# Performance work log

Measured on AMD Instinct MI355X. Metric: run time of the kernel, lower is better.

## Reference

```python
import jax, jax.numpy as jnp
import numpy as np

T, N, E = 8, 10000, 200000
F_IN, H, OUT = 32, 128, 64
EPS = 1e-5


def setup_inputs() -> dict:
    key = jax.random.key(0)
    ks = jax.random.split(key, 28)
    inp = {}
    inp['x'] = jax.random.normal(ks[0], (T, N, F_IN), jnp.float32)
    inp['edge_index'] = jax.random.randint(ks[1], (2, E), 0, N, dtype=jnp.int32)
    # GCN layer weights (Glorot-ish scale)
    inp['w_gcn0'] = jax.random.normal(ks[2], (F_IN, H), jnp.float32) / np.float32(np.sqrt(F_IN))
    inp['b_gcn0'] = jnp.zeros((H,), jnp.float32)
    inp['w_gcn1'] = jax.random.normal(ks[3], (H, H), jnp.float32) / np.float32(np.sqrt(H))
    inp['b_gcn1'] = jnp.zeros((H,), jnp.float32)
    inp['w_gcn2'] = jax.random.normal(ks[4], (H, H), jnp.float32) / np.float32(np.sqrt(H))
    inp['b_gcn2'] = jnp.zeros((H,), jnp.float32)
    # BatchNorm (eval mode) params for the two inner norms
    for i, kb in zip(range(2), range(5, 9, 2)):
        inp[f'bn_g{i}'] = 1.0 + 0.1 * jax.random.normal(ks[kb], (H,), jnp.float32)
        inp[f'bn_b{i}'] = 0.1 * jax.random.normal(ks[kb + 1], (H,), jnp.float32)
        inp[f'bn_m{i}'] = 0.1 * jax.random.normal(ks[kb + 10], (H,), jnp.float32)
        inp[f'bn_v{i}'] = jax.random.uniform(ks[kb + 11], (H,), jnp.float32, 0.5, 1.5)
    # 3-layer LSTM params, torch gate order (i, f, g, o)
    s = np.float32(1.0 / np.sqrt(OUT))
    dims_in = [H, OUT, OUT]
    for l in range(3):
        k0, k1, k2, k3 = jax.random.split(ks[20 + l], 4)
        inp[f'w_ih_{l}'] = jax.random.uniform(k0, (4 * OUT, dims_in[l]), jnp.float32, -s, s)
        inp[f'w_hh_{l}'] = jax.random.uniform(k1, (4 * OUT, OUT), jnp.float32, -s, s)
        inp[f'b_ih_{l}'] = jax.random.uniform(k2, (4 * OUT,), jnp.float32, -s, s)
        inp[f'b_hh_{l}'] = jax.random.uniform(k3, (4 * OUT,), jnp.float32, -s, s)
    return inp


def reference(x, edge_index, w_gcn0, b_gcn0, w_gcn1, b_gcn1, w_gcn2, b_gcn2,
              bn_g0, bn_b0, bn_m0, bn_v0, bn_g1, bn_b1, bn_m1, bn_v1,
              w_ih_0, w_hh_0, b_ih_0, b_hh_0,
              w_ih_1, w_hh_1, b_ih_1, b_hh_1,
              w_ih_2, w_hh_2, b_ih_2, b_hh_2):
    src, dst = edge_index[0], edge_index[1]
    # symmetric GCN normalization with self-loops: deg = in-degree + 1
    deg = jax.ops.segment_sum(jnp.ones((E,), x.dtype), dst, num_segments=N) + 1.0
    dis = jax.lax.rsqrt(deg)
    coef = dis[src] * dis[dst]          # [E] edge norm
    self_w = dis * dis                   # [N] self-loop norm

    def gcn(h, W, b):
        hw = jnp.einsum('tnf,fo->tno', h, W)                      # [T,N,O]
        msg = hw[:, src, :] * coef[None, :, None]                  # [T,E,O]
        agg = jax.vmap(lambda m: jax.ops.segment_sum(m, dst, num_segments=N))(msg)
        return agg + hw * self_w[None, :, None] + b

    def bn(h, g, b_, m, v):  # eval-mode BatchNorm1d
        return (h - m) * (g * jax.lax.rsqrt(v + EPS)) + b_

    h = bn(jax.nn.relu(gcn(x, w_gcn0, b_gcn0)), bn_g0, bn_b0, bn_m0, bn_v0)
    h = bn(jax.nn.relu(gcn(h, w_gcn1, b_gcn1)), bn_g1, bn_b1, bn_m1, bn_v1)
    h = jax.nn.relu(gcn(h, w_gcn2, b_gcn2))                        # [T,N,H]

    def lstm_layer(xs, Wih, Whh, bih, bhh):
        Hd = Whh.shape[1]
        bias = bih + bhh
        def step(carry, xt):
            hp, cp = carry
            g = xt @ Wih.T + hp @ Whh.T + bias
            i, f, gg, o = jnp.split(g, 4, axis=-1)
            c = jax.nn.sigmoid(f) * cp + jax.nn.sigmoid(i) * jnp.tanh(gg)
            hn = jax.nn.sigmoid(o) * jnp.tanh(c)
            return (hn, c), hn
        z = jnp.zeros((xs.shape[1], Hd), xs.dtype)
        _, ys = jax.lax.scan(step, (z, z), xs)
        return ys  # [T,N,Hd]

    ys = lstm_layer(h, w_ih_0, w_hh_0, b_ih_0, b_hh_0)
    ys = lstm_layer(ys, w_ih_1, w_hh_1, b_ih_1, b_hh_1)
    ys = lstm_layer(ys, w_ih_2, w_hh_2, b_ih_2, b_hh_2)
    return ys[-1]  # [N, OUT] == x[:, -1, :] in the torch code
```

## Files before the change

kernel.cpp:

```cpp
#include <hip/hip_runtime.h>
#include <hip/hip_bf16.h>
#include <math.h>

#define NTHREADS 256
#define T_STEPS 8
#define F_INC 32
#define H_DIM 128
#define O_DIM 64

typedef unsigned short u16;
typedef __attribute__((ext_vector_type(8))) short short8_t;
typedef __attribute__((ext_vector_type(4))) float float4_t;
typedef __attribute__((ext_vector_type(2))) float float2_t;

__device__ __forceinline__ float bf2f(u16 u) {
    return __uint_as_float(((unsigned)u) << 16);
}
__device__ __forceinline__ u16 f2bf(float f) {
    __hip_bfloat16 h = __float2bfloat16(f);
    union { __hip_bfloat16 h; u16 s; } cv; cv.h = h; return cv.s;
}
__device__ __forceinline__ float2_t bfpair(unsigned u) {
    union { unsigned w[2]; float2_t f; } c;
    c.w[0] = u << 16;
    c.w[1] = u & 0xffff0000u;
    return c.f;
}
__device__ __forceinline__ void bf8_unpack(uint4 u, float* f) {
    f[0] = __uint_as_float(u.x << 16); f[1] = __uint_as_float(u.x & 0xffff0000u);
    f[2] = __uint_as_float(u.y << 16); f[3] = __uint_as_float(u.y & 0xffff0000u);
    f[4] = __uint_as_float(u.z << 16); f[5] = __uint_as_float(u.z & 0xffff0000u);
    f[6] = __uint_as_float(u.w << 16); f[7] = __uint_as_float(u.w & 0xffff0000u);
}
__device__ __forceinline__ float fsig(float x) {
    float xc = fminf(fmaxf(x, -30.f), 30.f);
    float e = __builtin_amdgcn_exp2f(xc * -1.4426950408889634f);
    return __builtin_amdgcn_rcpf(1.0f + e);
}
__device__ __forceinline__ float ftanh(float x) {
    float xc = fminf(fmaxf(x, -15.f), 15.f);
    float e = __builtin_amdgcn_exp2f(xc * -2.8853900817779268f);
    float r = __builtin_amdgcn_rcpf(1.0f + e);
    return fmaf(-2.0f * e, r, 1.0f);
}

__global__ void count_wprep_kernel(const int* __restrict__ ei, int* __restrict__ cnt,
                                   int E, int gE,
                                   const float* g0, const float* g1, const float* g2,
                                   const float* i0, const float* i1, const float* i2,
                                   const float* h0, const float* h1, const float* h2,
                                   u16* o_g0, u16* o_g1, u16* o_g2,
                                   u16* o_i0, u16* o_i1, u16* o_i2,
                                   u16* o_h0, u16* o_h1, u16* o_h2) {
    if ((int)blockIdx.x < gE) {
        int e = blockIdx.x * NTHREADS + threadIdx.x;
        if (e < E) atomicAdd(&cnt[ei[E + e]], 1);
        return;
    }
    const int i = (blockIdx.x - gE) * NTHREADS + threadIdx.x;
    if (i < 4096)        { o_g0[i] = f2bf(g0[(i & 31) * 128 + (i >> 5)]); }
    else if (i < 20480)  { int j = i - 4096;   o_g1[j] = f2bf(g1[(j & 127) * 128 + (j >> 7)]); }
    else if (i < 36864)  { int j = i - 20480;  o_g2[j] = f2bf(g2[(j & 127) * 128 + (j >> 7)]); }
    else if (i < 69632)  { int j = i - 36864;  o_i0[j] = f2bf(i0[j]); }
    else if (i < 86016)  { int j = i - 69632;  o_i1[j] = f2bf(i1[j]); }
    else if (i < 102400) { int j = i - 86016;  o_i2[j] = f2bf(i2[j]); }
    else if (i < 118784) { int j = i - 102400; o_h0[j] = f2bf(h0[j]); }
    else if (i < 135168) { int j = i - 118784; o_h1[j] = f2bf(h1[j]); }
    else if (i < 151552) { int j = i - 135168; o_h2[j] = f2bf(h2[j]); }
}

__global__ void scan_part1(const int* __restrict__ cnt, int* __restrict__ bsum, int n) {
    __shared__ int sd[NTHREADS];
    const int i = blockIdx.x * NTHREADS + threadIdx.x;
    sd[threadIdx.x] = (i < n) ? cnt[i] : 0;
    __syncthreads();
    for (int off = 128; off > 0; off >>= 1) {
        if (threadIdx.x < off) sd[threadIdx.x] += sd[threadIdx.x + off];
        __syncthreads();
    }
    if (threadIdx.x == 0) bsum[blockIdx.x] = sd[0];
}

__global__ void scan_part3(const int* __restrict__ cnt, const int* __restrict__ bsum,
                           int* __restrict__ rowptr, int* __restrict__ wp,
                           float* __restrict__ dis, float* __restrict__ selfw, int n) {
    __shared__ int sd[NTHREADS];
    __shared__ int sbase;
    const int tid = threadIdx.x;
    if (tid < 64) {
        int v0 = (tid < blockIdx.x) ? bsum[tid] : 0;
        #pragma unroll
        for (int off = 1; off < 64; off <<= 1) v0 += __shfl_xor(v0, off);
        if (tid == 0) sbase = v0;
    }
    const int i = blockIdx.x * NTHREADS + tid;
    const int v = (i < n) ? cnt[i] : 0;
    sd[tid] = v;
    __syncthreads();
    for (int off = 1; off < NTHREADS; off <<= 1) {
        const int tv = (tid >= off) ? sd[tid - off] : 0;
        __syncthreads();
        sd[tid] += tv;
        __syncthreads();
    }
    const int excl = sbase + sd[tid] - v;
    if (i < n) {
        rowptr[i] = excl; wp[i] = excl;
        if (i == n - 1) rowptr[n] = excl + v;
        const float d = 1.0f + (float)v;
        dis[i] = rsqrtf(d);
        selfw[i] = 1.0f / d;
    }
}

__global__ void fill_kernel(const int* __restrict__ ei, const float* __restrict__ dis,
                            int* __restrict__ wp, int2* __restrict__ epk, int E) {
    int e = blockIdx.x * NTHREADS + threadIdx.x;
    if (e < E) {
        int s = ei[e], d = ei[E + e];
        int p = atomicAdd(&wp[d], 1);
        epk[p] = make_int2(s, __float_as_int(dis[s] * dis[d]));
    }
}

__global__ __launch_bounds__(NTHREADS)
void gcn32_kernel(const float* __restrict__ x, const int* __restrict__ rowptr,
                  const int2* __restrict__ epk,
                  const float* __restrict__ selfw, const u16* __restrict__ Wt,
                  const float* __restrict__ bias,
                  const float* __restrict__ bng, const float* __restrict__ bnb,
                  const float* __restrict__ bnm, const float* __restrict__ bnv,
                  u16* __restrict__ out, int N) {
    constexpr int ASTR = 40;
    constexpr int ECAP = 1024;
    __shared__ __align__(16) u16 aT[2][16][ASTR];
    __shared__ int2 sM[ECAP];
    const int t0 = blockIdx.x * 2;
    const int n0 = blockIdx.y * 16;
    const int tid = threadIdx.x;
    const int wid = tid >> 6, lane = tid & 63;
    const int quad = lane >> 4, l16 = lane & 15;
    const float* xb0 = x + (long)t0 * N * 32;
    const float* xb1 = xb0 + (long)N * 32;

    const int eb0 = rowptr[n0];
    const int ecnt = min(rowptr[n0 + 16] - eb0, ECAP);
    for (int p = tid; p < ecnt; p += NTHREADS) sM[p] = epk[eb0 + p];
    __syncthreads();

    const int split = lane >> 3;
    const int c4 = (lane & 7) * 4;
    for (int i = 0; i < 4; ++i) {
        const int n = n0 + wid * 4 + i;
        const int l0 = rowptr[n] - eb0;
        const int l1 = rowptr[n + 1] - eb0;
        const int eL = min(l1, ecnt);
        const int start = l0 + split;
        float2_t a0[2] = {(float2_t){0.f, 0.f}, (float2_t){0.f, 0.f}};
        float2_t a1[2] = {(float2_t){0.f, 0.f}, (float2_t){0.f, 0.f}};
        #pragma unroll 2
        for (int e = start; e < eL; e += 8) {
            const int2 m = sM[e];
            const float w = __int_as_float(m.y);
            const float2_t w2 = {w, w};
            const long o = (long)m.x * 32 + c4;
            const float4 v0 = *(const float4*)(xb0 + o);
            const float4 v1 = *(const float4*)(xb1 + o);
            a0[0] = __builtin_elementwise_fma((float2_t){v0.x, v0.y}, w2, a0[0]);
            a0[1] = __builtin_elementwise_fma((float2_t){v0.z, v0.w}, w2, a0[1]);
            a1[0] = __builtin_elementwise_fma((float2_t){v1.x, v1.y}, w2, a1[0]);
            a1[1] = __builtin_elementwise_fma((float2_t){v1.z, v1.w}, w2, a1[1]);
        }
        const int kL = (eL > start) ? (eL - start + 7) >> 3 : 0;
        for (int e = start + kL * 8; e < l1; e += 8) {
            const int2 m = epk[eb0 + e];
            const float w = __int_as_float(m.y);
            const float2_t w2 = {w, w};
            const long o = (long)m.x * 32 + c4;
            const float4 v0 = *(const float4*)(xb0 + o);
            const float4 v1 = *(const float4*)(xb1 + o);
            a0[0] = __builtin_elementwise_fma((float2_t){v0.x, v0.y}, w2, a0[0]);
            a0[1] = __builtin_elementwise_fma((float2_t){v0.z, v0.w}, w2, a0[1]);
            a1[0] = __builtin_elementwise_fma((float2_t){v1.x, v1.y}, w2, a1[0]);
            a1[1] = __builtin_elementwise_fma((float2_t){v1.z, v1.w}, w2, a1[1]);
        }
        float r[8] = {a0[0][0], a0[0][1], a0[1][0], a0[1][1],
                      a1[0][0], a1[0][1], a1[1][0], a1[1][1]};
        #pragma unroll
        for (int j = 0; j < 8; ++j) {
            r[j] += __shfl_xor(r[j], 8);
            r[j] += __shfl_xor(r[j], 16);
            r[j] += __shfl_xor(r[j], 32);
        }
        if (split == 0) {
            const float sw = selfw[n];
            const float4 s0 = *(const float4*)(xb0 + (long)n * 32 + c4);
            const float4 s1 = *(const float4*)(xb1 + (long)n * 32 + c4);
            ushort4 o0, o1;
            o0.x = f2bf(fmaf(sw, s0.x, r[0])); o0.y = f2bf(fmaf(sw, s0.y, r[1]));
            o0.z = f2bf(fmaf(sw, s0.z, r[2])); o0.w = f2bf(fmaf(sw, s0.w, r[3]));
            o1.x = f2bf(fmaf(sw, s1.x, r[4])); o1.y = f2bf(fmaf(sw, s1.y, r[5]));
            o1.z = f2bf(fmaf(sw, s1.z, r[6])); o1.w = f2bf(fmaf(sw, s1.w, r[7]));
            *(ushort4*)(&aT[0][wid * 4 + i][c4]) = o0;
            *(ushort4*)(&aT[1][wid * 4 + i][c4]) = o1;
        }
    }
    __syncthreads();

    const short8_t fA0 = *(const short8_t*)(&aT[0][l16][quad * 8]);
    const short8_t fA1 = *(const short8_t*)(&aT[1][l16][quad * 8]);
    float4_t acc[2][2];
    short8_t fB[2];
    #pragma unroll
    for (int ct = 0; ct < 2; ++ct) {
        const int col = wid * 32 + ct * 16 + l16;
        fB[ct] = *(const short8_t*)(Wt + (long)col * 32 + quad * 8);
        acc[0][ct] = (float4_t){0.f, 0.f, 0.f, 0.f};
        acc[1][ct] = (float4_t){0.f, 0.f, 0.f, 0.f};
    }
    #pragma unroll
    for (int ct = 0; ct < 2; ++ct) {
        acc[0][ct] = __builtin_amdgcn_mfma_f32_16x16x32_bf16(fA0, fB[ct], acc[0][ct], 0, 0, 0);
        acc[1][ct] = __builtin_amdgcn_mfma_f32_16x16x32_bf16(fA1, fB[ct], acc[1][ct], 0, 0, 0);
    }

    #pragma unroll
    for (int ct = 0; ct < 2; ++ct) {
        const int c = wid * 32 + ct * 16 + l16;
        const float s = bng[c] * rsqrtf(bnv[c] + 1e-5f);
        const float a1 = bnb[c] - bnm[c] * s;
        const float a0 = bias[c];
        #pragma unroll
        for (int tt = 0; tt < 2; ++tt) {
            #pragma unroll
            for (int r = 0; r < 4; ++r) {
                const int node = quad * 4 + r;
                float v = fmaf(fmaxf(acc[tt][ct][r] + a0, 0.f), s, a1);
                out[((long)(t0 + tt) * N + n0 + node) * 128 + c] = f2bf(v);
            }
        }
    }
}

template<int EPI>
__global__ __launch_bounds__(NTHREADS)
void gcn128_kernel(const u16* __restrict__ h, const int* __restrict__ rowptr,
                   const int2* __restrict__ epk,
                   const float* __restrict__ selfw, const u16* __restrict__ Wt,
                   const float* __restrict__ bias,
                   const float* __restrict__ bng, const float* __restrict__ bnb,
                   const float* __restrict__ bnm, const float* __restrict__ bnv,
                   u16* __restrict__ out, int N) {
    constexpr int ASTR = 136;
    constexpr int ECAP = 1024;
    __shared__ __align__(16) u16 aT[2][16][ASTR];
    __shared__ int2 sM[ECAP];
    const int t0 = blockIdx.x * 2;
    const int n0 = blockIdx.y * 16;
    const int tid = threadIdx.x;
    const int wid = tid >> 6, lane = tid & 63;
    const int quad = lane >> 4, l16 = lane & 15;
    const u16* hb0 = h + (long)t0 * N * 128;
    const u16* hb1 = hb0 + (long)N * 128;

    const int eb0 = rowptr[n0];
    const int ecnt = min(rowptr[n0 + 16] - eb0, ECAP);
    for (int p = tid; p < ecnt; p += NTHREADS) sM[p] = epk[eb0 + p];
    __syncthreads();

    const int split = lane >> 4;
    const int c8 = l16 * 8;
    for (int i = 0; i < 4; ++i) {
        const int n = n0 + wid * 4 + i;
        const int l0 = rowptr[n] - eb0;
        const int l1 = rowptr[n + 1] - eb0;
        const int eL = min(l1, ecnt);
        const int start = l0 + split;
        float2_t aA[4] = {(float2_t){0.f, 0.f}, (float2_t){0.f, 0.f},
                          (float2_t){0.f, 0.f}, (float2_t){0.f, 0.f}};
        float2_t aB[4] = {(float2_t){0.f, 0.f}, (float2_t){0.f, 0.f},
                          (float2_t){0.f, 0.f}, (float2_t){0.f, 0.f}};
        #pragma unroll 4
        for (int e = start; e < eL; e += 4) {
            const int2 m = sM[e];
            const float w = __int_as_float(m.y);
            const float2_t w2 = {w, w};
            const long o = (long)m.x * 128 + c8;
            const uint4 v0 = *(const uint4*)(hb0 + o);
            const uint4 v1 = *(const uint4*)(hb1 + o);
            aA[0] = __builtin_elementwise_fma(bfpair(v0.x), w2, aA[0]);
            aA[1] = __builtin_elementwise_fma(bfpair(v0.y), w2, aA[1]);
            aA[2] = __builtin_elementwise_fma(bfpair(v0.z), w2, aA[2]);
            aA[3] = __builtin_elementwise_fma(bfpair(v0.w), w2, aA[3]);
            aB[0] = __builtin_elementwise_fma(bfpair(v1.x), w2, aB[0]);
            aB[1] = __builtin_elementwise_fma(bfpair(v1.y), w2, aB[1]);
            aB[2] = __builtin_elementwise_fma(bfpair(v1.z), w2, aB[2]);
            aB[3] = __builtin_elementwise_fma(bfpair(v1.w), w2, aB[3]);
        }
        const int kL = (eL > start) ? (eL - start + 3) >> 2 : 0;
        for (int e = start + kL * 4; e < l1; e += 4) {
            const int2 m = epk[eb0 + e];
            const float w = __int_as_float(m.y);
            const float2_t w2 = {w, w};
            const long o = (long)m.x * 128 + c8;
            const uint4 v0 = *(const uint4*)(hb0 + o);
            const uint4 v1 = *(const uint4*)(hb1 + o);
            aA[0] = __builtin_elementwise_fma(bfpair(v0.x), w2, aA[0]);
            aA[1] = __builtin_elementwise_fma(bfpair(v0.y), w2, aA[1]);
            aA[2] = __builtin_elementwise_fma(bfpair(v0.z), w2, aA[2]);
            aA[3] = __builtin_elementwise_fma(bfpair(v0.w), w2, aA[3]);
            aB[0] = __builtin_elementwise_fma(bfpair(v1.x), w2, aB[0]);
            aB[1] = __builtin_elementwise_fma(bfpair(v1.y), w2, aB[1]);
            aB[2] = __builtin_elementwise_fma(bfpair(v1.z), w2, aB[2]);
            aB[3] = __builtin_elementwise_fma(bfpair(v1.w), w2, aB[3]);
        }
        float a[16] = {aA[0][0], aA[0][1], aA[1][0], aA[1][1],
                       aA[2][0], aA[2][1], aA[3][0], aA[3][1],
                       aB[0][0], aB[0][1], aB[1][0], aB[1][1],
                       aB[2][0], aB[2][1], aB[3][0], aB[3][1]};
        #pragma unroll
        for (int j = 0; j < 16; ++j) {
            a[j] += __shfl_xor(a[j], 16);
            a[j] += __shfl_xor(a[j], 32);
        }
        if (split == 0) {
            const float sw = selfw[n];
            const uint4 s0 = *(const uint4*)(hb0 + (long)n * 128 + c8);
            const uint4 s1 = *(const uint4*)(hb1 + (long)n * 128 + c8);
            float f0[8], f1[8];
            bf8_unpack(s0, f0);
            bf8_unpack(s1, f1);
            ushort4 oA0, oA1, oB0, oB1;
            oA0.x = f2bf(fmaf(sw, f0[0], a[0]));  oA0.y = f2bf(fmaf(sw, f0[1], a[1]));
            oA0.z = f2bf(fmaf(sw, f0[2], a[2]));  oA0.w = f2bf(fmaf(sw, f0[3], a[3]));
            oA1.x = f2bf(fmaf(sw, f0[4], a[4]));  oA1.y = f2bf(fmaf(sw, f0[5], a[5]));
            oA1.z = f2bf(fmaf(sw, f0[6], a[6]));  oA1.w = f2bf(fmaf(sw, f0[7], a[7]));
            oB0.x = f2bf(fmaf(sw, f1[0], a[8]));  oB0.y = f2bf(fmaf(sw, f1[1], a[9]));
            oB0.z = f2bf(fmaf(sw, f1[2], a[10])); oB0.w = f2bf(fmaf(sw, f1[3], a[11]));
            oB1.x = f2bf(fmaf(sw, f1[4], a[12])); oB1.y = f2bf(fmaf(sw, f1[5], a[13]));
            oB1.z = f2bf(fmaf(sw, f1[6], a[14])); oB1.w = f2bf(fmaf(sw, f1[7], a[15]));
            *(ushort4*)(&aT[0][wid * 4 + i][c8]) = oA0;
            *(ushort4*)(&aT[0][wid * 4 + i][c8 + 4]) = oA1;
            *(ushort4*)(&aT[1][wid * 4 + i][c8]) = oB0;
            *(ushort4*)(&aT[1][wid * 4 + i][c8 + 4]) = oB1;
        }
    }
    __syncthreads();

    short8_t fA0[4], fA1[4];
    #pragma unroll
    for (int ks = 0; ks < 4; ++ks) {
        fA0[ks] = *(const short8_t*)(&aT[0][l16][ks * 32 + quad * 8]);
        fA1[ks] = *(const short8_t*)(&aT[1][l16][ks * 32 + quad * 8]);
    }
    float4_t acc[2][2];
    #pragma unroll
    for (int tt = 0; tt < 2; ++tt)
        #pragma unroll
        for (int ct = 0; ct < 2; ++ct) acc[tt][ct] = (float4_t){0.f, 0.f, 0.f, 0.f};
    #pragma unroll
    for (int ct = 0; ct < 2; ++ct) {
        const int col = wid * 32 + ct * 16 + l16;
        #pragma unroll
        for (int ks = 0; ks < 4; ++ks) {
            const short8_t fB = *(const short8_t*)(Wt + (long)col * 128 + ks * 32 + quad * 8);
            acc[0][ct] = __builtin_amdgcn_mfma_f32_16x16x32_bf16(fA0[ks], fB, acc[0][ct], 0, 0, 0);
            acc[1][ct] = __builtin_amdgcn_mfma_f32_16x16x32_bf16(fA1[ks], fB, acc[1][ct], 0, 0, 0);
        }
    }

    #pragma unroll
    for (int ct = 0; ct < 2; ++ct) {
        const int c = wid * 32 + ct * 16 + l16;
        const float a0 = bias[c];
        float s = 0.f, a1 = 0.f;
        if constexpr (EPI == 2) {
            s = bng[c] * rsqrtf(bnv[c] + 1e-5f);
            a1 = bnb[c] - bnm[c] * s;
        }
        #pragma unroll
        for (int tt = 0; tt < 2; ++tt) {
            #pragma unroll
            for (int r = 0; r < 4; ++r) {
                const int node = quad * 4 + r;
                float v = fmaxf(acc[tt][ct][r] + a0, 0.f);
                if constexpr (EPI == 2) v = fmaf(v, s, a1);
                out[((long)(t0 + tt) * N + n0 + node) * 128 + c] = f2bf(v);
            }
        }
    }
}

__global__ __launch_bounds__(NTHREADS, 2)
void lstm0_kernel(const u16* __restrict__ in_h, const u16* __restrict__ wih,
                  const u16* __restrict__ whh,
                  const float* __restrict__ bi, const float* __restrict__ bh,
                  u16* __restrict__ out_hi, u16* __restrict__ out_lo, int N) {
    constexpr int HSTR = 76;
    const int tid = threadIdx.x;
    const int w = tid >> 6, lane = tid & 63;
    const int quad = lane >> 4, l16 = lane & 15;
    const int n0 = blockIdx.x * 16;
    const int u = w * 16 + l16;

    __shared__ __align__(16) u16 hT[2][16][HSTR];
    for (int p = tid; p < 2 * 16 * HSTR; p += NTHREADS) (&hT[0][0][0])[p] = 0;

    short8_t fI[4][4], fH[4][2];
    #pragma unroll
    for (int g = 0; g < 4; ++g) {
        #pragma unroll
        for (int ks = 0; ks < 4; ++ks)
            fI[g][ks] = *(const short8_t*)(wih + (long)(g * 64 + u) * 128 + ks * 32 + quad * 8);
        #pragma unroll
        for (int ks = 0; ks < 2; ++ks)
            fH[g][ks] = *(const short8_t*)(whh + (long)(g * 64 + u) * 64 + ks * 32 + quad * 8);
    }
    float bias[4];
    #pragma unroll
    for (int g = 0; g < 4; ++g) bias[g] = bi[g * 64 + u] + bh[g * 64 + u];
    float cst[4] = {};
    __syncthreads();

    #pragma unroll 1
    for (int t = 0; t < T_STEPS; ++t) {
        short8_t ain[4];
        const long ibase = ((long)t * N + n0 + l16) * 128 + quad * 8;
        #pragma unroll
        for (int ks = 0; ks < 4; ++ks)
            ain[ks] = *(const short8_t*)(in_h + ibase + ks * 32);
        short8_t ah[2], al[2];
        #pragma unroll
        for (int ks = 0; ks < 2; ++ks) {
            ah[ks] = *(const short8_t*)(&hT[0][l16][ks * 32 + quad * 8]);
            al[ks] = *(const short8_t*)(&hT[1][l16][ks * 32 + quad * 8]);
        }
        __syncthreads();

        float4_t acc[4];
        #pragma unroll
        for (int g = 0; g < 4; ++g) acc[g] = (float4_t){bias[g], bias[g], bias[g], bias[g]};
        #pragma unroll
        for (int ks = 0; ks < 4; ++ks)
            #pragma unroll
            for (int g = 0; g < 4; ++g)
                acc[g] = __builtin_amdgcn_mfma_f32_16x16x32_bf16(ain[ks], fI[g][ks], acc[g], 0, 0, 0);
        #pragma unroll
        for (int ks = 0; ks < 2; ++ks)
            #pragma unroll
            for (int g = 0; g < 4; ++g) {
                acc[g] = __builtin_amdgcn_mfma_f32_16x16x32_bf16(ah[ks], fH[g][ks], acc[g], 0, 0, 0);
                acc[g] = __builtin_amdgcn_mfma_f32_16x16x32_bf16(al[ks], fH[g][ks], acc[g], 0, 0, 0);
            }

        #pragma unroll
        for (int r = 0; r < 4; ++r) {
            const float si = fsig(acc[0][r]);
            const float sf = fsig(acc[1][r]);
            const float gg = ftanh(acc[2][r]);
            const float so = fsig(acc[3][r]);
            const float c = sf * cst[r] + si * gg;
            cst[r] = c;
            const float h = so * ftanh(c);
            const int node = quad * 4 + r;
            const u16 hi = f2bf(h);
            const u16 lo = f2bf(h - bf2f(hi));
            hT[0][node][u] = hi;
            hT[1][node][u] = lo;
            const long o = ((long)t * N + n0 + node) * 64 + u;
            out_hi[o] = hi;
            out_lo[o] = lo;
        }
        __syncthreads();
    }
}

__global__ __launch_bounds__(NTHREADS)
void lstm12_kernel(const u16* __restrict__ in_hi, const u16* __restrict__ in_lo,
                   const u16* __restrict__ wih1, const u16* __restrict__ whh1,
                   const u16* __restrict__ wih2, const u16* __restrict__ whh2,
                   const float* __restrict__ bi1, const float* __restrict__ bh1,
                   const float* __restrict__ bi2, const float* __restrict__ bh2,
                   float* __restrict__ out_f, int N) {
    constexpr int HSTR = 76;
    const int tid = threadIdx.x;
    const int w = tid >> 6, lane = tid & 63;
    const int quad = lane >> 4, l16 = lane & 15;
    const int n0 = blockIdx.x * 16;
    const int u = w * 16 + l16;

    __shared__ __align__(16) u16 hT[2][2][16][HSTR];
    for (int p = tid; p < 2 * 2 * 16 * HSTR; p += NTHREADS) (&hT[0][0][0][0])[p] = 0;

    short8_t fI1[4][2], fH1[4][2], fI2[4][2], fH2[4][2];
    #pragma unroll
    for (int g = 0; g < 4; ++g)
        #pragma unroll
        for (int ks = 0; ks < 2; ++ks) {
            fI1[g][ks] = *(const short8_t*)(wih1 + (long)(g * 64 + u) * 64 + ks * 32 + quad * 8);
            fH1[g][ks] = *(const short8_t*)(whh1 + (long)(g * 64 + u) * 64 + ks * 32 + quad * 8);
            fI2[g][ks] = *(const short8_t*)(wih2 + (long)(g * 64 + u) * 64 + ks * 32 + quad * 8);
            fH2[g][ks] = *(const short8_t*)(whh2 + (long)(g * 64 + u) * 64 + ks * 32 + quad * 8);
        }
    float b1[4], b2[4];
    #pragma unroll
    for (int g = 0; g < 4; ++g) {
        b1[g] = bi1[g * 64 + u] + bh1[g * 64 + u];
        b2[g] = bi2[g * 64 + u] + bh2[g * 64 + u];
    }
    float c1[4] = {}, c2[4] = {};
    __syncthreads();

    #pragma unroll 1
    for (int t = 0; t < T_STEPS; ++t) {
        short8_t ainh[2], ainl[2], r1h[2], r1l[2], r2h[2], r2l[2];
        const long ibase = ((long)t * N + n0 + l16) * 64 + quad * 8;
        #pragma unroll
        for (int ks = 0; ks < 2; ++ks) {
            ainh[ks] = *(const short8_t*)(in_hi + ibase + ks * 32);
            ainl[ks] = *(const short8_t*)(in_lo + ibase + ks * 32);
            r1h[ks] = *(const short8_t*)(&hT[0][0][l16][ks * 32 + quad * 8]);
            r1l[ks] = *(const short8_t*)(&hT[0][1][l16][ks * 32 + quad * 8]);
            r2h[ks] = *(const short8_t*)(&hT[1][0][l16][ks * 32 + quad * 8]);
            r2l[ks] = *(const short8_t*)(&hT[1][1][l16][ks * 32 + quad * 8]);
        }
        __syncthreads();

        float4_t acc[4];
        #pragma unroll
        for (int g = 0; g < 4; ++g) acc[g] = (float4_t){b1[g], b1[g], b1[g], b1[g]};
        #pragma unroll
        for (int ks = 0; ks < 2; ++ks)
            #pragma unroll
            for (int g = 0; g < 4; ++g) {
                acc[g] = __builtin_amdgcn_mfma_f32_16x16x32_bf16(ainh[ks], fI1[g][ks], acc[g], 0, 0, 0);
                acc[g] = __builtin_amdgcn_mfma_f32_16x16x32_bf16(ainl[ks], fI1[g][ks], acc[g], 0, 0, 0);
                acc[g] = __builtin_amdgcn_mfma_f32_16x16x32_bf16(r1h[ks], fH1[g][ks], acc[g], 0, 0, 0);
                acc[g] = __builtin_amdgcn_mfma_f32_16x16x32_bf16(r1l[ks], fH1[g][ks], acc[g], 0, 0, 0);
            }
        #pragma unroll
        for (int r = 0; r < 4; ++r) {
            const float si = fsig(acc[0][r]);
            const float sf = fsig(acc[1][r]);
            const float gg = ftanh(acc[2][r]);
            const float so = fsig(acc[3][r]);
            const float c = sf * c1[r] + si * gg;
            c1[r] = c;
            const float h = so * ftanh(c);
            const int node = quad * 4 + r;
            const u16 hi = f2bf(h);
            hT[0][0][node][u] = hi;
            hT[0][1][node][u] = f2bf(h - bf2f(hi));
        }
        __syncthreads();

        short8_t i2h[2], i2l[2];
        #pragma unroll
        for (int ks = 0; ks < 2; ++ks) {
            i2h[ks] = *(const short8_t*)(&hT[0][0][l16][ks * 32 + quad * 8]);
            i2l[ks] = *(const short8_t*)(&hT[0][1][l16][ks * 32 + quad * 8]);
        }
        #pragma unroll
        for (int g = 0; g < 4; ++g) acc[g] = (float4_t){b2[g], b2[g], b2[g], b2[g]};
        #pragma unroll
        for (int ks = 0; ks < 2; ++ks)
            #pragma unroll
            for (int g = 0; g < 4; ++g) {
                acc[g] = __builtin_amdgcn_mfma_f32_16x16x32_bf16(i2h[ks], fI2[g][ks], acc[g], 0, 0, 0);
                acc[g] = __builtin_amdgcn_mfma_f32_16x16x32_bf16(i2l[ks], fI2[g][ks], acc[g], 0, 0, 0);
                acc[g] = __builtin_amdgcn_mfma_f32_16x16x32_bf16(r2h[ks], fH2[g][ks], acc[g], 0, 0, 0);
                acc[g] = __builtin_amdgcn_mfma_f32_16x16x32_bf16(r2l[ks], fH2[g][ks], acc[g], 0, 0, 0);
            }
        #pragma unroll
        for (int r = 0; r < 4; ++r) {
            const float si = fsig(acc[0][r]);
            const float sf = fsig(acc[1][r]);
            const float gg = ftanh(acc[2][r]);
            const float so = fsig(acc[3][r]);
            const float c = sf * c2[r] + si * gg;
            c2[r] = c;
            const float h = so * ftanh(c);
            const int node = quad * 4 + r;
            if (t == T_STEPS - 1) {
                out_f[(long)(n0 + node) * 64 + u] = h;
            } else {
                const u16 hi = f2bf(h);
                hT[1][0][node][u] = hi;
                hT[1][1][node][u] = f2bf(h - bf2f(hi));
            }
        }
        __syncthreads();
    }
}

extern "C" void kernel_launch(void* const* d_in, const int* in_sizes, int n_in,
                              void* d_out, int out_size, void* d_ws, size_t ws_size,
                              hipStream_t stream) {
    (void)n_in; (void)out_size; (void)ws_size;
    const float* x      = (const float*)d_in[0];
    const int*   ei     = (const int*)d_in[1];
    const float* w_gcn0 = (const float*)d_in[2];
    const float* b_gcn0 = (const float*)d_in[3];
    const float* w_gcn1 = (const float*)d_in[4];
    const float* b_gcn1 = (const float*)d_in[5];
    const float* w_gcn2 = (const float*)d_in[6];
    const float* b_gcn2 = (const float*)d_in[7];
    const float* bn_g0  = (const float*)d_in[8];
    const float* bn_b0  = (const float*)d_in[9];
    const float* bn_m0  = (const float*)d_in[10];
    const float* bn_v0  = (const float*)d_in[11];
    const float* bn_g1  = (const float*)d_in[12];
    const float* bn_b1  = (const float*)d_in[13];
    const float* bn_m1  = (const float*)d_in[14];
    const float* bn_v1  = (const float*)d_in[15];
    const float* w_ih_0 = (const float*)d_in[16];
    const float* w_hh_0 = (const float*)d_in[17];
    const float* b_ih_0 = (const float*)d_in[18];
    const float* b_hh_0 = (const float*)d_in[19];
    const float* w_ih_1 = (const float*)d_in[20];
    const float* w_hh_1 = (const float*)d_in[21];
    const float* b_ih_1 = (const float*)d_in[22];
    const float* b_hh_1 = (const float*)d_in[23];
    const float* w_ih_2 = (const float*)d_in[24];
    const float* w_hh_2 = (const float*)d_in[25];
    const float* b_ih_2 = (const float*)d_in[26];
    const float* b_hh_2 = (const float*)d_in[27];

    const int E = in_sizes[1] / 2;
    const int N = in_sizes[0] / (T_STEPS * F_INC);
    const long M = (long)N * T_STEPS;

    char* ws = (char*)d_ws;
    size_t off = 0;
    auto carve = [&](size_t bytes) -> void* {
        void* p = ws + off;
        off += (bytes + 255) & ~(size_t)255;
        return p;
    };
    float* dis     = (float*)carve((size_t)N * 4);
    float* selfw   = (float*)carve((size_t)N * 4);
    int*   cnt     = (int*)carve((size_t)N * 4);
    int*   rowptr  = (int*)carve((size_t)(N + 1) * 4);
    int*   wp      = (int*)carve((size_t)N * 4);
    int2*  epk     = (int2*)carve((size_t)E * 8);
    int*   bsum    = (int*)carve(64 * 4);
    u16*   hbuf    = (u16*)carve((size_t)M * H_DIM * 2);
    u16*   hbuf2   = (u16*)carve((size_t)M * H_DIM * 2);
    u16*   pA_hi   = (u16*)carve((size_t)M * O_DIM * 2);
    u16*   pA_lo   = (u16*)carve((size_t)M * O_DIM * 2);
    u16*   wt0     = (u16*)carve((size_t)128 * 32 * 2);
    u16*   wt1     = (u16*)carve((size_t)128 * 128 * 2);
    u16*   wt2     = (u16*)carve((size_t)128 * 128 * 2);
    u16*   wtih0   = (u16*)carve((size_t)256 * 128 * 2);
    u16*   wtih1   = (u16*)carve((size_t)256 * 64 * 2);
    u16*   wtih2   = (u16*)carve((size_t)256 * 64 * 2);
    u16*   whh0b   = (u16*)carve((size_t)256 * 64 * 2);
    u16*   whh1b   = (u16*)carve((size_t)256 * 64 * 2);
    u16*   whh2b   = (u16*)carve((size_t)256 * 64 * 2);

    const dim3 b256(NTHREADS);
    const int gN = (N + NTHREADS - 1) / NTHREADS;
    const int gE = (E + NTHREADS - 1) / NTHREADS;

    hipMemsetAsync(cnt, 0, (size_t)N * 4, stream);
    count_wprep_kernel<<<gE + (151552 + 255) / 256, b256, 0, stream>>>(
        ei, cnt, E, gE,
        w_gcn0, w_gcn1, w_gcn2, w_ih_0, w_ih_1, w_ih_2, w_hh_0, w_hh_1, w_hh_2,
        wt0, wt1, wt2, wtih0, wtih1, wtih2, whh0b, whh1b, whh2b);
    scan_part1<<<gN, b256, 0, stream>>>(cnt, bsum, N);
    scan_part3<<<gN, b256, 0, stream>>>(cnt, bsum, rowptr, wp, dis, selfw, N);
    fill_kernel<<<gE, b256, 0, stream>>>(ei, dis, wp, epk, E);

    const dim3 gG(T_STEPS / 2, N / 16);
    gcn32_kernel<<<gG, b256, 0, stream>>>(
        x, rowptr, epk, selfw, wt0, b_gcn0,
        bn_g0, bn_b0, bn_m0, bn_v0, hbuf, N);
    gcn128_kernel<2><<<gG, b256, 0, stream>>>(
        hbuf, rowptr, epk, selfw, wt1, b_gcn1,
        bn_g1, bn_b1, bn_m1, bn_v1, hbuf2, N);
    gcn128_kernel<1><<<gG, b256, 0, stream>>>(
        hbuf2, rowptr, epk, selfw, wt2, b_gcn2,
        nullptr, nullptr, nullptr, nullptr, hbuf, N);

    const int gL = N / 16;
    lstm0_kernel<<<gL, b256, 0, stream>>>(
        hbuf, wtih0, whh0b, b_ih_0, b_hh_0, pA_hi, pA_lo, N);
    lstm12_kernel<<<gL, b256, 0, stream>>>(
        pA_hi, pA_lo, wtih1, whh1b, wtih2, whh2b,
        b_ih_1, b_hh_1, b_ih_2, b_hh_2, (float*)d_out, N);
}
```

Measured before the change: 363.8 us.

## Convert x to bf16 upfront and split gcn128 blocks to one timestep

The prep kernel gains extra blocks that convert the fp32 input x to bf16, so the first GCN layer gathers half as many bytes per neighbor, and its gather loop unroll goes from 2 to 4. The 128-wide GCN kernels now handle one timestep per block instead of two, doubling the grid and halving per-thread registers and accumulators to raise occupancy and parallelism. The costs are an extra pass over x with a new workspace buffer, bf16 rounding of the raw input, and edge metadata that is now loaded twice as often in the 128-wide layers.

```diff
diff --git a/kernel.cpp b/kernel.cpp
--- a/kernel.cpp
+++ b/kernel.cpp
@@ -45,7 +45,8 @@
 }
 
 __global__ void count_wprep_kernel(const int* __restrict__ ei, int* __restrict__ cnt,
-                                   int E, int gE,
+                                   int E, int gE, int NX,
+                                   const float* __restrict__ x, u16* __restrict__ xb,
                                    const float* g0, const float* g1, const float* g2,
                                    const float* i0, const float* i1, const float* i2,
                                    const float* h0, const float* h1, const float* h2,
@@ -57,16 +58,26 @@
         if (e < E) atomicAdd(&cnt[ei[E + e]], 1);
         return;
     }
-    const int i = (blockIdx.x - gE) * NTHREADS + threadIdx.x;
-    if (i < 4096)        { o_g0[i] = f2bf(g0[(i & 31) * 128 + (i >> 5)]); }
-    else if (i < 20480)  { int j = i - 4096;   o_g1[j] = f2bf(g1[(j & 127) * 128 + (j >> 7)]); }
-    else if (i < 36864)  { int j = i - 20480;  o_g2[j] = f2bf(g2[(j & 127) * 128 + (j >> 7)]); }
-    else if (i < 69632)  { int j = i - 36864;  o_i0[j] = f2bf(i0[j]); }
-    else if (i < 86016)  { int j = i - 69632;  o_i1[j] = f2bf(i1[j]); }
-    else if (i < 102400) { int j = i - 86016;  o_i2[j] = f2bf(i2[j]); }
-    else if (i < 118784) { int j = i - 102400; o_h0[j] = f2bf(h0[j]); }
-    else if (i < 135168) { int j = i - 118784; o_h1[j] = f2bf(h1[j]); }
-    else if (i < 151552) { int j = i - 135168; o_h2[j] = f2bf(h2[j]); }
+    if ((int)blockIdx.x < gE + 592) {
+        const int i = (blockIdx.x - gE) * NTHREADS + threadIdx.x;
+        if (i < 4096)        { o_g0[i] = f2bf(g0[(i & 31) * 128 + (i >> 5)]); }
+        else if (i < 20480)  { int j = i - 4096;   o_g1[j] = f2bf(g1[(j & 127) * 128 + (j >> 7)]); }
+        else if (i < 36864)  { int j = i - 20480;  o_g2[j] = f2bf(g2[(j & 127) * 128 + (j >> 7)]); }
+        else if (i < 69632)  { int j = i - 36864;  o_i0[j] = f2bf(i0[j]); }
+        else if (i < 86016)  { int j = i - 69632;  o_i1[j] = f2bf(i1[j]); }
+        else if (i < 102400) { int j = i - 86016;  o_i2[j] = f2bf(i2[j]); }
+        else if (i < 118784) { int j = i - 102400; o_h0[j] = f2bf(h0[j]); }
+        else if (i < 135168) { int j = i - 118784; o_h1[j] = f2bf(h1[j]); }
+        else if (i < 151552) { int j = i - 135168; o_h2[j] = f2bf(h2[j]); }
+        return;
+    }
+    const long i4 = ((long)(blockIdx.x - gE - 592) * NTHREADS + threadIdx.x) * 4;
+    if (i4 < (long)NX) {
+        const float4 v = *(const float4*)(x + i4);
+        ushort4 o;
+        o.x = f2bf(v.x); o.y = f2bf(v.y); o.z = f2bf(v.z); o.w = f2bf(v.w);
+        *(ushort4*)(xb + i4) = o;
+    }
 }
 
 __global__ void scan_part1(const int* __restrict__ cnt, int* __restrict__ bsum, int n) {
@@ -124,7 +135,7 @@
 }
 
 __global__ __launch_bounds__(NTHREADS)
-void gcn32_kernel(const float* __restrict__ x, const int* __restrict__ rowptr,
+void gcn32_kernel(const u16* __restrict__ xb, const int* __restrict__ rowptr,
                   const int2* __restrict__ epk,
                   const float* __restrict__ selfw, const u16* __restrict__ Wt,
                   const float* __restrict__ bias,
@@ -140,8 +151,8 @@
     const int tid = threadIdx.x;
     const int wid = tid >> 6, lane = tid & 63;
     const int quad = lane >> 4, l16 = lane & 15;
-    const float* xb0 = x + (long)t0 * N * 32;
-    const float* xb1 = xb0 + (long)N * 32;
+    const u16* xb0 = xb + (long)t0 * N * 32;
+    const u16* xb1 = xb0 + (long)N * 32;
 
     const int eb0 = rowptr[n0];
     const int ecnt = min(rowptr[n0 + 16] - eb0, ECAP);
@@ -158,18 +169,18 @@
         const int start = l0 + split;
         float2_t a0[2] = {(float2_t){0.f, 0.f}, (float2_t){0.f, 0.f}};
         float2_t a1[2] = {(float2_t){0.f, 0.f}, (float2_t){0.f, 0.f}};
-        #pragma unroll 2
+        #pragma unroll 4
         for (int e = start; e < eL; e += 8) {
             const int2 m = sM[e];
             const float w = __int_as_float(m.y);
             const float2_t w2 = {w, w};
             const long o = (long)m.x * 32 + c4;
-            const float4 v0 = *(const float4*)(xb0 + o);
-            const float4 v1 = *(const float4*)(xb1 + o);
-            a0[0] = __builtin_elementwise_fma((float2_t){v0.x, v0.y}, w2, a0[0]);
-            a0[1] = __builtin_elementwise_fma((float2_t){v0.z, v0.w}, w2, a0[1]);
-            a1[0] = __builtin_elementwise_fma((float2_t){v1.x, v1.y}, w2, a1[0]);
-            a1[1] = __builtin_elementwise_fma((float2_t){v1.z, v1.w}, w2, a1[1]);
+            const uint2 v0 = *(const uint2*)(xb0 + o);
+            const uint2 v1 = *(const uint2*)(xb1 + o);
+            a0[0] = __builtin_elementwise_fma(bfpair(v0.x), w2, a0[0]);
+            a0[1] = __builtin_elementwise_fma(bfpair(v0.y), w2, a0[1]);
+            a1[0] = __builtin_elementwise_fma(bfpair(v1.x), w2, a1[0]);
+            a1[1] = __builtin_elementwise_fma(bfpair(v1.y), w2, a1[1]);
         }
         const int kL = (eL > start) ? (eL - start + 7) >> 3 : 0;
         for (int e = start + kL * 8; e < l1; e += 8) {
@@ -177,12 +188,12 @@
             const float w = __int_as_float(m.y);
             const float2_t w2 = {w, w};
             const long o = (long)m.x * 32 + c4;
-            const float4 v0 = *(const float4*)(xb0 + o);
-            const float4 v1 = *(const float4*)(xb1 + o);
-            a0[0] = __builtin_elementwise_fma((float2_t){v0.x, v0.y}, w2, a0[0]);
-            a0[1] = __builtin_elementwise_fma((float2_t){v0.z, v0.w}, w2, a0[1]);
-            a1[0] = __builtin_elementwise_fma((float2_t){v1.x, v1.y}, w2, a1[0]);
-            a1[1] = __builtin_elementwise_fma((float2_t){v1.z, v1.w}, w2, a1[1]);
+            const uint2 v0 = *(const uint2*)(xb0 + o);
+            const uint2 v1 = *(const uint2*)(xb1 + o);
+            a0[0] = __builtin_elementwise_fma(bfpair(v0.x), w2, a0[0]);
+            a0[1] = __builtin_elementwise_fma(bfpair(v0.y), w2, a0[1]);
+            a1[0] = __builtin_elementwise_fma(bfpair(v1.x), w2, a1[0]);
+            a1[1] = __builtin_elementwise_fma(bfpair(v1.y), w2, a1[1]);
         }
         float r[8] = {a0[0][0], a0[0][1], a0[1][0], a0[1][1],
                       a1[0][0], a1[0][1], a1[1][0], a1[1][1]};
@@ -194,13 +205,15 @@
         }
         if (split == 0) {
             const float sw = selfw[n];
-            const float4 s0 = *(const float4*)(xb0 + (long)n * 32 + c4);
-            const float4 s1 = *(const float4*)(xb1 + (long)n * 32 + c4);
+            const uint2 s0 = *(const uint2*)(xb0 + (long)n * 32 + c4);
+            const uint2 s1 = *(const uint2*)(xb1 + (long)n * 32 + c4);
+            const float2_t s0a = bfpair(s0.x), s0b = bfpair(s0.y);
+            const float2_t s1a = bfpair(s1.x), s1b = bfpair(s1.y);
             ushort4 o0, o1;
-            o0.x = f2bf(fmaf(sw, s0.x, r[0])); o0.y = f2bf(fmaf(sw, s0.y, r[1]));
-            o0.z = f2bf(fmaf(sw, s0.z, r[2])); o0.w = f2bf(fmaf(sw, s0.w, r[3]));
-            o1.x = f2bf(fmaf(sw, s1.x, r[4])); o1.y = f2bf(fmaf(sw, s1.y, r[5]));
-            o1.z = f2bf(fmaf(sw, s1.z, r[6])); o1.w = f2bf(fmaf(sw, s1.w, r[7]));
+            o0.x = f2bf(fmaf(sw, s0a[0], r[0])); o0.y = f2bf(fmaf(sw, s0a[1], r[1]));
+            o0.z = f2bf(fmaf(sw, s0b[0], r[2])); o0.w = f2bf(fmaf(sw, s0b[1], r[3]));
+            o1.x = f2bf(fmaf(sw, s1a[0], r[4])); o1.y = f2bf(fmaf(sw, s1a[1], r[5]));
+            o1.z = f2bf(fmaf(sw, s1b[0], r[6])); o1.w = f2bf(fmaf(sw, s1b[1], r[7]));
             *(ushort4*)(&aT[0][wid * 4 + i][c4]) = o0;
             *(ushort4*)(&aT[1][wid * 4 + i][c4]) = o1;
         }
@@ -253,15 +266,14 @@
                    u16* __restrict__ out, int N) {
     constexpr int ASTR = 136;
     constexpr int ECAP = 1024;
-    __shared__ __align__(16) u16 aT[2][16][ASTR];
+    __shared__ __align__(16) u16 aT[16][ASTR];
     __shared__ int2 sM[ECAP];
-    const int t0 = blockIdx.x * 2;
+    const int t = blockIdx.x;
     const int n0 = blockIdx.y * 16;
     const int tid = threadIdx.x;
     const int wid = tid >> 6, lane = tid & 63;
     const int quad = lane >> 4, l16 = lane & 15;
-    const u16* hb0 = h + (long)t0 * N * 128;
-    const u16* hb1 = hb0 + (long)N * 128;
+    const u16* hb = h + (long)t * N * 128;
 
     const int eb0 = rowptr[n0];
     const int ecnt = min(rowptr[n0 + 16] - eb0, ECAP);
@@ -276,96 +288,67 @@
         const int l1 = rowptr[n + 1] - eb0;
         const int eL = min(l1, ecnt);
         const int start = l0 + split;
-        float2_t aA[4] = {(float2_t){0.f, 0.f}, (float2_t){0.f, 0.f},
-                          (float2_t){0.f, 0.f}, (float2_t){0.f, 0.f}};
-        float2_t aB[4] = {(float2_t){0.f, 0.f}, (float2_t){0.f, 0.f},
+        float2_t a2[4] = {(float2_t){0.f, 0.f}, (float2_t){0.f, 0.f},
                           (float2_t){0.f, 0.f}, (float2_t){0.f, 0.f}};
         #pragma unroll 4
         for (int e = start; e < eL; e += 4) {
             const int2 m = sM[e];
             const float w = __int_as_float(m.y);
             const float2_t w2 = {w, w};
-            const long o = (long)m.x * 128 + c8;
-            const uint4 v0 = *(const uint4*)(hb0 + o);
-            const uint4 v1 = *(const uint4*)(hb1 + o);
-            aA[0] = __builtin_elementwise_fma(bfpair(v0.x), w2, aA[0]);
-            aA[1] = __builtin_elementwise_fma(bfpair(v0.y), w2, aA[1]);
-            aA[2] = __builtin_elementwise_fma(bfpair(v0.z), w2, aA[2]);
-            aA[3] = __builtin_elementwise_fma(bfpair(v0.w), w2, aA[3]);
-            aB[0] = __builtin_elementwise_fma(bfpair(v1.x), w2, aB[0]);
-            aB[1] = __builtin_elementwise_fma(bfpair(v1.y), w2, aB[1]);
-            aB[2] = __builtin_elementwise_fma(bfpair(v1.z), w2, aB[2]);
-            aB[3] = __builtin_elementwise_fma(bfpair(v1.w), w2, aB[3]);
+            const uint4 v = *(const uint4*)(hb + (long)m.x * 128 + c8);
+            a2[0] = __builtin_elementwise_fma(bfpair(v.x), w2, a2[0]);
+            a2[1] = __builtin_elementwise_fma(bfpair(v.y), w2, a2[1]);
+            a2[2] = __builtin_elementwise_fma(bfpair(v.z), w2, a2[2]);
+            a2[3] = __builtin_elementwise_fma(bfpair(v.w), w2, a2[3]);
         }
         const int kL = (eL > start) ? (eL - start + 3) >> 2 : 0;
         for (int e = start + kL * 4; e < l1; e += 4) {
             const int2 m = epk[eb0 + e];
             const float w = __int_as_float(m.y);
             const float2_t w2 = {w, w};
-            const long o = (long)m.x * 128 + c8;
-            const uint4 v0 = *(const uint4*)(hb0 + o);
-            const uint4 v1 = *(const uint4*)(hb1 + o);
-            aA[0] = __builtin_elementwise_fma(bfpair(v0.x), w2, aA[0]);
-            aA[1] = __builtin_elementwise_fma(bfpair(v0.y), w2, aA[1]);
-            aA[2] = __builtin_elementwise_fma(bfpair(v0.z), w2, aA[2]);
-            aA[3] = __builtin_elementwise_fma(bfpair(v0.w), w2, aA[3]);
-            aB[0] = __builtin_elementwise_fma(bfpair(v1.x), w2, aB[0]);
-            aB[1] = __builtin_elementwise_fma(bfpair(v1.y), w2, aB[1]);
-            aB[2] = __builtin_elementwise_fma(bfpair(v1.z), w2, aB[2]);
-            aB[3] = __builtin_elementwise_fma(bfpair(v1.w), w2, aB[3]);
-        }
-        float a[16] = {aA[0][0], aA[0][1], aA[1][0], aA[1][1],
-                       aA[2][0], aA[2][1], aA[3][0], aA[3][1],
-                       aB[0][0], aB[0][1], aB[1][0], aB[1][1],
-                       aB[2][0], aB[2][1], aB[3][0], aB[3][1]};
-        #pragma unroll
-        for (int j = 0; j < 16; ++j) {
+            const uint4 v = *(const uint4*)(hb + (long)m.x * 128 + c8);
+            a2[0] = __builtin_elementwise_fma(bfpair(v.x), w2, a2[0]);
+            a2[1] = __builtin_elementwise_fma(bfpair(v.y), w2, a2[1]);
+            a2[2] = __builtin_elementwise_fma(bfpair(v.z), w2, a2[2]);
+            a2[3] = __builtin_elementwise_fma(bfpair(v.w), w2, a2[3]);
+        }
+        float a[8] = {a2[0][0], a2[0][1], a2[1][0], a2[1][1],
+                      a2[2][0], a2[2][1], a2[3][0], a2[3][1]};
+        #pragma unroll
+        for (int j = 0; j < 8; ++j) {
             a[j] += __shfl_xor(a[j], 16);
             a[j] += __shfl_xor(a[j], 32);
         }
         if (split == 0) {
             const float sw = selfw[n];
-            const uint4 s0 = *(const uint4*)(hb0 + (long)n * 128 + c8);
-            const uint4 s1 = *(const uint4*)(hb1 + (long)n * 128 + c8);
-            float f0[8], f1[8];
-            bf8_unpack(s0, f0);
-            bf8_unpack(s1, f1);
-            ushort4 oA0, oA1, oB0, oB1;
-            oA0.x = f2bf(fmaf(sw, f0[0], a[0]));  oA0.y = f2bf(fmaf(sw, f0[1], a[1]));
-            oA0.z = f2bf(fmaf(sw, f0[2], a[2]));  oA0.w = f2bf(fmaf(sw, f0[3], a[3]));
-            oA1.x = f2bf(fmaf(sw, f0[4], a[4]));  oA1.y = f2bf(fmaf(sw, f0[5], a[5]));
-            oA1.z = f2bf(fmaf(sw, f0[6], a[6]));  oA1.w = f2bf(fmaf(sw, f0[7], a[7]));
-            oB0.x = f2bf(fmaf(sw, f1[0], a[8]));  oB0.y = f2bf(fmaf(sw, f1[1], a[9]));
-            oB0.z = f2bf(fmaf(sw, f1[2], a[10])); oB0.w = f2bf(fmaf(sw, f1[3], a[11]));
-            oB1.x = f2bf(fmaf(sw, f1[4], a[12])); oB1.y = f2bf(fmaf(sw, f1[5], a[13]));
-            oB1.z = f2bf(fmaf(sw, f1[6], a[14])); oB1.w = f2bf(fmaf(sw, f1[7], a[15]));
-            *(ushort4*)(&aT[0][wid * 4 + i][c8]) = oA0;
-            *(ushort4*)(&aT[0][wid * 4 + i][c8 + 4]) = oA1;
-            *(ushort4*)(&aT[1][wid * 4 + i][c8]) = oB0;
-            *(ushort4*)(&aT[1][wid * 4 + i][c8 + 4]) = oB1;
-        }
-    }
-    __syncthreads();
-
-    short8_t fA0[4], fA1[4];
-    #pragma unroll
-    for (int ks = 0; ks < 4; ++ks) {
-        fA0[ks] = *(const short8_t*)(&aT[0][l16][ks * 32 + quad * 8]);
-        fA1[ks] = *(const short8_t*)(&aT[1][l16][ks * 32 + quad * 8]);
-    }
-    float4_t acc[2][2];
-    #pragma unroll
-    for (int tt = 0; tt < 2; ++tt)
-        #pragma unroll
-        for (int ct = 0; ct < 2; ++ct) acc[tt][ct] = (float4_t){0.f, 0.f, 0.f, 0.f};
+            const uint4 sv = *(const uint4*)(hb + (long)n * 128 + c8);
+            float f[8];
+            bf8_unpack(sv, f);
+            ushort4 o0, o1;
+            o0.x = f2bf(fmaf(sw, f[0], a[0])); o0.y = f2bf(fmaf(sw, f[1], a[1]));
+            o0.z = f2bf(fmaf(sw, f[2], a[2])); o0.w = f2bf(fmaf(sw, f[3], a[3]));
+            o1.x = f2bf(fmaf(sw, f[4], a[4])); o1.y = f2bf(fmaf(sw, f[5], a[5]));
+            o1.z = f2bf(fmaf(sw, f[6], a[6])); o1.w = f2bf(fmaf(sw, f[7], a[7]));
+            *(ushort4*)(&aT[wid * 4 + i][c8]) = o0;
+            *(ushort4*)(&aT[wid * 4 + i][c8 + 4]) = o1;
+        }
+    }
+    __syncthreads();
+
+    short8_t fA[4];
+    #pragma unroll
+    for (int ks = 0; ks < 4; ++ks)
+        fA[ks] = *(const short8_t*)(&aT[l16][ks * 32 + quad * 8]);
+    float4_t acc[2];
+    #pragma unroll
+    for (int ct = 0; ct < 2; ++ct) acc[ct] = (float4_t){0.f, 0.f, 0.f, 0.f};
     #pragma unroll
     for (int ct = 0; ct < 2; ++ct) {
         const int col = wid * 32 + ct * 16 + l16;
         #pragma unroll
         for (int ks = 0; ks < 4; ++ks) {
             const short8_t fB = *(const short8_t*)(Wt + (long)col * 128 + ks * 32 + quad * 8);
-            acc[0][ct] = __builtin_amdgcn_mfma_f32_16x16x32_bf16(fA0[ks], fB, acc[0][ct], 0, 0, 0);
-            acc[1][ct] = __builtin_amdgcn_mfma_f32_16x16x32_bf16(fA1[ks], fB, acc[1][ct], 0, 0, 0);
+            acc[ct] = __builtin_amdgcn_mfma_f32_16x16x32_bf16(fA[ks], fB, acc[ct], 0, 0, 0);
         }
     }
 
@@ -379,14 +362,11 @@
             a1 = bnb[c] - bnm[c] * s;
         }
         #pragma unroll
-        for (int tt = 0; tt < 2; ++tt) {
-            #pragma unroll
-            for (int r = 0; r < 4; ++r) {
-                const int node = quad * 4 + r;
-                float v = fmaxf(acc[tt][ct][r] + a0, 0.f);
-                if constexpr (EPI == 2) v = fmaf(v, s, a1);
-                out[((long)(t0 + tt) * N + n0 + node) * 128 + c] = f2bf(v);
-            }
+        for (int r = 0; r < 4; ++r) {
+            const int node = quad * 4 + r;
+            float v = fmaxf(acc[ct][r] + a0, 0.f);
+            if constexpr (EPI == 2) v = fmaf(v, s, a1);
+            out[((long)t * N + n0 + node) * 128 + c] = f2bf(v);
         }
     }
 }
@@ -644,6 +624,7 @@
     int*   wp      = (int*)carve((size_t)N * 4);
     int2*  epk     = (int2*)carve((size_t)E * 8);
     int*   bsum    = (int*)carve(64 * 4);
+    u16*   xb      = (u16*)carve((size_t)M * F_INC * 2);
     u16*   hbuf    = (u16*)carve((size_t)M * H_DIM * 2);
     u16*   hbuf2   = (u16*)carve((size_t)M * H_DIM * 2);
     u16*   pA_hi   = (u16*)carve((size_t)M * O_DIM * 2);
@@ -661,20 +642,22 @@
     const dim3 b256(NTHREADS);
     const int gN = (N + NTHREADS - 1) / NTHREADS;
     const int gE = (E + NTHREADS - 1) / NTHREADS;
+    const int NX = (int)(M * F_INC);
+    const int gX = (NX / 4 + NTHREADS - 1) / NTHREADS;
 
     hipMemsetAsync(cnt, 0, (size_t)N * 4, stream);
-    count_wprep_kernel<<<gE + (151552 + 255) / 256, b256, 0, stream>>>(
-        ei, cnt, E, gE,
+    count_wprep_kernel<<<gE + 592 + gX, b256, 0, stream>>>(
+        ei, cnt, E, gE, NX, x, xb,
         w_gcn0, w_gcn1, w_gcn2, w_ih_0, w_ih_1, w_ih_2, w_hh_0, w_hh_1, w_hh_2,
         wt0, wt1, wt2, wtih0, wtih1, wtih2, whh0b, whh1b, whh2b);
     scan_part1<<<gN, b256, 0, stream>>>(cnt, bsum, N);
     scan_part3<<<gN, b256, 0, stream>>>(cnt, bsum, rowptr, wp, dis, selfw, N);
     fill_kernel<<<gE, b256, 0, stream>>>(ei, dis, wp, epk, E);
 
-    const dim3 gG(T_STEPS / 2, N / 16);
-    gcn32_kernel<<<gG, b256, 0, stream>>>(
-        x, rowptr, epk, selfw, wt0, b_gcn0,
+    gcn32_kernel<<<dim3(T_STEPS / 2, N / 16), b256, 0, stream>>>(
+        xb, rowptr, epk, selfw, wt0, b_gcn0,
         bn_g0, bn_b0, bn_m0, bn_v0, hbuf, N);
+    const dim3 gG(T_STEPS, N / 16);
     gcn128_kernel<2><<<gG, b256, 0, stream>>>(
         hbuf, rowptr, epk, selfw, wt1, b_gcn1,
         bn_g1, bn_b1, bn_m1, bn_v1, hbuf2, N);
```

Result: faster. 354.4 us (-2.6%).
